# Optimization experiments

Measured on AMD Instinct MI355X. Metric: run time of the kernel, lower is better.

## Reference

```python
import jax, jax.numpy as jnp
import numpy as np

HEADS = 8


def _proj(inp, W, b):
    # 1x1 conv == per-pixel dense: W [Cout, Cin], inp [B, Cin, H, W]
    return jnp.einsum('oc,bchw->bohw', W, inp) + b[None, :, None, None]


def setup_inputs() -> dict:
    key = jax.random.key(0)
    ks = jax.random.split(key, 10)
    B, C, H, W = 2, 256, 64, 64
    s = 0.02
    return {
        'x': jax.random.normal(ks[0], (B, C, H, W), jnp.float32),
        'f_lu': jax.random.normal(ks[1], (B, C, H, W), jnp.float32),
        'Wq': jax.random.normal(ks[2], (C, C), jnp.float32) * s,
        'bq': jnp.zeros((C,), jnp.float32),
        'Wk': jax.random.normal(ks[3], (C, C), jnp.float32) * s,
        'bk': jnp.zeros((C,), jnp.float32),
        'Wv': jax.random.normal(ks[4], (C, C), jnp.float32) * s,
        'bv': jnp.zeros((C,), jnp.float32),
        'Wo': jax.random.normal(ks[5], (C, C), jnp.float32) * s,
        'bo': jnp.zeros((C,), jnp.float32),
    }


def reference(x, f_lu, Wq, bq, Wk, bk, Wv, bv, Wo, bo):
    b, c, h, w = x.shape
    heads = HEADS
    dk = c // heads
    scale = dk ** (-0.5)
    hw = h * w

    def to_heads(t):
        # [b, c, h, w] -> [b, heads, hw, dk]
        return t.reshape(b, heads, dk, hw).transpose(0, 1, 3, 2)

    q = to_heads(_proj(f_lu, Wq, bq))
    k = to_heads(_proj(x, Wk, bk))
    v = to_heads(_proj(x, Wv, bv))

    attn = jnp.einsum('bhnd,bhmd->bhnm', q, k) * scale  # [b, heads, hw, hw]
    attn = jax.nn.softmax(attn, axis=-1)
    out = jnp.einsum('bhnm,bhmd->bhnd', attn, v)  # [b, heads, hw, dk]
    out = out.transpose(0, 1, 3, 2).reshape(b, c, h, w)
    return _proj(out, Wo, bo)
```

## Files before the change

### kernel.cpp

```cpp
#include <hip/hip_runtime.h>

typedef __bf16 bf16_t;
typedef bf16_t bf16x8 __attribute__((ext_vector_type(8)));
typedef bf16_t bf16x4 __attribute__((ext_vector_type(4)));
typedef float f32x4 __attribute__((ext_vector_type(4)));

#define HW 4096
#define NC 256

__device__ __forceinline__ f32x4 mfma16(bf16x8 a, bf16x8 b, f32x4 c) {
  return __builtin_amdgcn_mfma_f32_16x16x32_bf16(a, b, c, 0, 0, 0);
}

__device__ __forceinline__ bf16x8 pack_bf16x8(float a0, float a1, float a2, float a3,
                                              float a4, float a5, float a6, float a7) {
  union { unsigned int u[4]; bf16x8 v; } r;
  asm("v_cvt_pk_bf16_f32 %0, %1, %2" : "=v"(r.u[0]) : "v"(a0), "v"(a1));
  asm("v_cvt_pk_bf16_f32 %0, %1, %2" : "=v"(r.u[1]) : "v"(a2), "v"(a3));
  asm("v_cvt_pk_bf16_f32 %0, %1, %2" : "=v"(r.u[2]) : "v"(a4), "v"(a5));
  asm("v_cvt_pk_bf16_f32 %0, %1, %2" : "=v"(r.u[3]) : "v"(a6), "v"(a7));
  return r.v;
}

__device__ __forceinline__ int kswz(int m) {
  return ((m >> 1) & 1) | (((m >> 3) & 1) << 1);
}

__global__ void cvt_w(const float* __restrict__ wq, const float* __restrict__ wk,
                      const float* __restrict__ wv, const float* __restrict__ wo,
                      bf16_t* __restrict__ dst) {
  int i = blockIdx.x * 256 + threadIdx.x;
  dst[i]          = (bf16_t)wq[i];
  dst[65536 + i]  = (bf16_t)wk[i];
  dst[131072 + i] = (bf16_t)wv[i];
  dst[196608 + i] = (bf16_t)wo[i];
}

__global__ __launch_bounds__(256) void proj_qkv(
    const float* __restrict__ x, const float* __restrict__ flu,
    const bf16_t* __restrict__ Wq, const bf16_t* __restrict__ Wk,
    const bf16_t* __restrict__ Wv,
    const float* __restrict__ bq, const float* __restrict__ bk,
    const float* __restrict__ bv,
    bf16_t* __restrict__ Qb, bf16_t* __restrict__ Kb, bf16_t* __restrict__ Vb) {
  const int p0 = blockIdx.x * 64;
  const int o0 = blockIdx.y * 64;
  const int b  = blockIdx.z;
  const int tid = threadIdx.x;
  const int w = tid >> 6;
  const int lane = tid & 63;
  const int ln = lane & 15, hi = lane >> 4;

  __shared__ __align__(16) bf16_t lds_f[64][40];
  __shared__ __align__(16) bf16_t lds_x[64][40];

  f32x4 accQ[4] = {}, accK[4] = {}, accV[4] = {};

  const int cl = tid >> 3;
  const int pp = (tid & 7) * 4;
  const float* fbase = flu + (size_t)b * NC * HW + p0;
  const float* xbase = x   + (size_t)b * NC * HW + p0;

  for (int c0 = 0; c0 < NC; c0 += 32) {
    __syncthreads();
    {
      const float* fr = fbase + (size_t)(c0 + cl) * HW;
      const float* xr = xbase + (size_t)(c0 + cl) * HW;
      float4 fa = *(const float4*)(fr + pp);
      float4 fb = *(const float4*)(fr + pp + 32);
      float4 xa = *(const float4*)(xr + pp);
      float4 xb = *(const float4*)(xr + pp + 32);
      lds_f[pp + 0][cl] = (bf16_t)fa.x;  lds_f[pp + 1][cl] = (bf16_t)fa.y;
      lds_f[pp + 2][cl] = (bf16_t)fa.z;  lds_f[pp + 3][cl] = (bf16_t)fa.w;
      lds_f[pp + 32][cl] = (bf16_t)fb.x; lds_f[pp + 33][cl] = (bf16_t)fb.y;
      lds_f[pp + 34][cl] = (bf16_t)fb.z; lds_f[pp + 35][cl] = (bf16_t)fb.w;
      lds_x[pp + 0][cl] = (bf16_t)xa.x;  lds_x[pp + 1][cl] = (bf16_t)xa.y;
      lds_x[pp + 2][cl] = (bf16_t)xa.z;  lds_x[pp + 3][cl] = (bf16_t)xa.w;
      lds_x[pp + 32][cl] = (bf16_t)xb.x; lds_x[pp + 33][cl] = (bf16_t)xb.y;
      lds_x[pp + 34][cl] = (bf16_t)xb.z; lds_x[pp + 35][cl] = (bf16_t)xb.w;
    }
    __syncthreads();

    bf16x8 af = *(const bf16x8*)&lds_f[w * 16 + ln][hi * 8];
    bf16x8 ax = *(const bf16x8*)&lds_x[w * 16 + ln][hi * 8];
    bf16x8 awv = *(const bf16x8*)(Wv + (size_t)(o0 + w * 16 + ln) * NC + c0 + hi * 8);
#pragma unroll
    for (int t = 0; t < 4; ++t) {
      bf16x8 bwq = *(const bf16x8*)(Wq + (size_t)(o0 + t * 16 + ln) * NC + c0 + hi * 8);
      accQ[t] = mfma16(af, bwq, accQ[t]);
      bf16x8 bwk = *(const bf16x8*)(Wk + (size_t)(o0 + t * 16 + ln) * NC + c0 + hi * 8);
      accK[t] = mfma16(ax, bwk, accK[t]);
      bf16x8 bx = *(const bf16x8*)&lds_x[t * 16 + ln][hi * 8];
      accV[t] = mfma16(awv, bx, accV[t]);
    }
  }

  const float scale = 0.17677669529663687f * 1.4426950408889634f;
#pragma unroll
  for (int t = 0; t < 4; ++t) {
    int o = o0 + t * 16 + ln;
    int h = o >> 5, d = o & 31;
    float bqv = bq[o], bkv = bk[o];
#pragma unroll
    for (int r = 0; r < 4; ++r) {
      int p = p0 + w * 16 + hi * 4 + r;
      size_t idx = (((size_t)(b * 8 + h)) * HW + p) * 32 + d;
      Qb[idx] = (bf16_t)((accQ[t][r] + bqv) * scale);
      Kb[idx] = (bf16_t)(accK[t][r] + bkv);
    }
  }
#pragma unroll
  for (int t = 0; t < 4; ++t) {
    int p = p0 + t * 16 + ln;
#pragma unroll
    for (int r = 0; r < 4; ++r) {
      int o = o0 + w * 16 + hi * 4 + r;
      Vb[((size_t)b * NC + o) * HW + p] = (bf16_t)(accV[t][r] + bv[o]);
    }
  }
}

__global__ __launch_bounds__(256, 2) void attn_fwd(
    const bf16_t* __restrict__ Qb, const bf16_t* __restrict__ Kb,
    const bf16_t* __restrict__ Vb, bf16_t* __restrict__ AO) {
  const int fid = blockIdx.y * 32 + blockIdx.x;
  const int lid = (fid & 7) * 64 + (fid >> 3);
  const int q0 = (lid & 31) * 128;
  const int bh = lid >> 5;
  const int b = bh >> 3, h = bh & 7;
  const int tid = threadIdx.x;
  const int w = tid >> 6, lane = tid & 63;
  const int ln = lane & 15, hi = lane >> 4;

  __shared__ __align__(16) bf16_t Kt[2][64 * 32];
  __shared__ __align__(16) bf16_t Vt[2][32 * 64];

  const bf16_t* Qh = Qb + (size_t)bh * HW * 32;
  const bf16_t* Kh = Kb + (size_t)bh * HW * 32;
  const bf16_t* Vh = Vb + ((size_t)b * NC + h * 32) * HW;

  const bf16x8 qf0 = *(const bf16x8*)(Qh + (size_t)(q0 + w * 32 + ln) * 32 + hi * 8);
  const bf16x8 qf1 = *(const bf16x8*)(Qh + (size_t)(q0 + w * 32 + 16 + ln) * 32 + hi * 8);

  f32x4 O[2][2] = {};
  f32x4 Lacc0 = {}, Lacc1 = {};
  const bf16_t one = (bf16_t)1.0f;
  const bf16x8 ones = {one, one, one, one, one, one, one, one};

  const int kr = tid >> 2, ks = tid & 3;
  const int kofs = kr * 32 + ((ks ^ kswz(kr)) * 8);
  const bf16_t* kgp = Kh + kr * 32 + ks * 8;

  const int vr = tid >> 3, vs = tid & 7;
  const int vofs = vr * 64 + ((vs ^ (vr & 7)) * 8);
  const bf16_t* vgp = Vh + (size_t)vr * HW + vs * 8;

  int kread[2][2];
  {
    const int F0 = 8 * (ln >> 2) + (ln & 3);
#pragma unroll
    for (int ch = 0; ch < 2; ++ch) {
#pragma unroll
      for (int j = 0; j < 2; ++j) {
        int row = ch * 32 + F0 + 4 * j;
        kread[ch][j] = row * 32 + ((hi ^ kswz(row)) * 8);
      }
    }
  }
  int vread[2][2];
#pragma unroll
  for (int dt = 0; dt < 2; ++dt)
#pragma unroll
    for (int ch = 0; ch < 2; ++ch)
      vread[dt][ch] = (dt * 16 + ln) * 64 + (((ch * 4 + hi) ^ (ln & 7)) * 8);

  bf16x8 kstA = *(const bf16x8*)kgp;
  bf16x8 vstA = *(const bf16x8*)vgp;
  bf16x8 kstB, vstB;

  auto compute = [&](const bf16_t* K_, const bf16_t* V_) {
    __builtin_amdgcn_s_setprio(1);
#pragma unroll
    for (int ch = 0; ch < 2; ++ch) {
      bf16x8 kf0 = *(const bf16x8*)&K_[kread[ch][0]];
      bf16x8 kf1 = *(const bf16x8*)&K_[kread[ch][1]];
      f32x4 z = {};
      f32x4 Sa0 = mfma16(kf0, qf0, z);
      f32x4 Sa1 = mfma16(kf1, qf0, z);
      f32x4 Sb0 = mfma16(kf0, qf1, z);
      f32x4 Sb1 = mfma16(kf1, qf1, z);
      float a0 = __builtin_amdgcn_exp2f(Sa0[0]), a1 = __builtin_amdgcn_exp2f(Sa0[1]);
      float a2 = __builtin_amdgcn_exp2f(Sa0[2]), a3 = __builtin_amdgcn_exp2f(Sa0[3]);
      float a4 = __builtin_amdgcn_exp2f(Sa1[0]), a5 = __builtin_amdgcn_exp2f(Sa1[1]);
      float a6 = __builtin_amdgcn_exp2f(Sa1[2]), a7 = __builtin_amdgcn_exp2f(Sa1[3]);
      float b0 = __builtin_amdgcn_exp2f(Sb0[0]), b1 = __builtin_amdgcn_exp2f(Sb0[1]);
      float b2 = __builtin_amdgcn_exp2f(Sb0[2]), b3 = __builtin_amdgcn_exp2f(Sb0[3]);
      float b4 = __builtin_amdgcn_exp2f(Sb1[0]), b5 = __builtin_amdgcn_exp2f(Sb1[1]);
      float b6 = __builtin_amdgcn_exp2f(Sb1[2]), b7 = __builtin_amdgcn_exp2f(Sb1[3]);
      bf16x8 pa = pack_bf16x8(a0, a1, a2, a3, a4, a5, a6, a7);
      bf16x8 pb = pack_bf16x8(b0, b1, b2, b3, b4, b5, b6, b7);
      Lacc0 = mfma16(ones, pa, Lacc0);
      Lacc1 = mfma16(ones, pb, Lacc1);
#pragma unroll
      for (int dt = 0; dt < 2; ++dt) {
        bf16x8 vf = *(const bf16x8*)&V_[vread[dt][ch]];
        O[0][dt] = mfma16(vf, pa, O[0][dt]);
        O[1][dt] = mfma16(vf, pb, O[1][dt]);
      }
    }
    __builtin_amdgcn_s_setprio(0);
  };

  for (int t = 0; t < 32; ++t) {
    *(bf16x8*)&Kt[0][kofs] = kstA;
    *(bf16x8*)&Vt[0][vofs] = vstA;
    __syncthreads();
    {
      kstB = *(const bf16x8*)(kgp + (size_t)(2 * t + 1) * 2048);
      vstB = *(const bf16x8*)(vgp + (2 * t + 1) * 64);
    }
    compute(Kt[0], Vt[0]);
    *(bf16x8*)&Kt[1][kofs] = kstB;
    *(bf16x8*)&Vt[1][vofs] = vstB;
    __syncthreads();
    if (t < 31) {
      kstA = *(const bf16x8*)(kgp + (size_t)(2 * t + 2) * 2048);
      vstA = *(const bf16x8*)(vgp + (2 * t + 2) * 64);
    }
    compute(Kt[1], Vt[1]);
  }

#pragma unroll
  for (int g = 0; g < 2; ++g) {
    float inv = 1.0f / (g ? Lacc1[0] : Lacc0[0]);
    const int p = q0 + w * 32 + g * 16 + ln;
#pragma unroll
    for (int dt = 0; dt < 2; ++dt) {
      f32x4 ov4 = O[g][dt];
      bf16x4 ov = {(bf16_t)(ov4[0] * inv), (bf16_t)(ov4[1] * inv),
                   (bf16_t)(ov4[2] * inv), (bf16_t)(ov4[3] * inv)};
      *(bf16x4*)(AO + ((size_t)b * HW + p) * NC + h * 32 + dt * 16 + hi * 4) = ov;
    }
  }
}

__global__ __launch_bounds__(256) void proj_out(
    const bf16_t* __restrict__ AO, const bf16_t* __restrict__ Wo,
    const float* __restrict__ bo, float* __restrict__ out) {
  const int p0 = blockIdx.x * 64;
  const int o0 = blockIdx.y * 64;
  const int b  = blockIdx.z;
  const int tid = threadIdx.x;
  const int w = tid >> 6, lane = tid & 63;
  const int ln = lane & 15, hi = lane >> 4;

  f32x4 acc[4] = {};
  for (int c0 = 0; c0 < NC; c0 += 32) {
    bf16x8 aw = *(const bf16x8*)(Wo + (size_t)(o0 + w * 16 + ln) * NC + c0 + hi * 8);
#pragma unroll
    for (int t = 0; t < 4; ++t) {
      bf16x8 bfr = *(const bf16x8*)(AO + ((size_t)b * HW + p0 + t * 16 + ln) * NC + c0 + hi * 8);
      acc[t] = mfma16(aw, bfr, acc[t]);
    }
  }
#pragma unroll
  for (int t = 0; t < 4; ++t) {
#pragma unroll
    for (int r = 0; r < 4; ++r) {
      int o = o0 + w * 16 + hi * 4 + r;
      out[((size_t)b * NC + o) * HW + p0 + t * 16 + ln] = acc[t][r] + bo[o];
    }
  }
}

extern "C" void kernel_launch(void* const* d_in, const int* in_sizes, int n_in,
                              void* d_out, int out_size, void* d_ws, size_t ws_size,
                              hipStream_t stream) {
  const float* x   = (const float*)d_in[0];
  const float* flu = (const float*)d_in[1];
  const float* Wq  = (const float*)d_in[2];
  const float* bq  = (const float*)d_in[3];
  const float* Wk  = (const float*)d_in[4];
  const float* bk  = (const float*)d_in[5];
  const float* Wv  = (const float*)d_in[6];
  const float* bv  = (const float*)d_in[7];
  const float* Wo  = (const float*)d_in[8];
  const float* bo  = (const float*)d_in[9];
  float* out = (float*)d_out;

  char* ws = (char*)d_ws;
  bf16_t* Qb = (bf16_t*)(ws);
  bf16_t* Kb = (bf16_t*)(ws + (4u << 20));
  bf16_t* Vb = (bf16_t*)(ws + (8u << 20));
  bf16_t* AO = (bf16_t*)(ws + (12u << 20));
  bf16_t* Wb = (bf16_t*)(ws + (16u << 20));

  cvt_w<<<256, 256, 0, stream>>>(Wq, Wk, Wv, Wo, Wb);
  proj_qkv<<<dim3(64, 4, 2), 256, 0, stream>>>(x, flu,
      Wb, Wb + 65536, Wb + 131072, bq, bk, bv, Qb, Kb, Vb);
  attn_fwd<<<dim3(32, 16), 256, 0, stream>>>(Qb, Kb, Vb, AO);
  proj_out<<<dim3(64, 4, 2), 256, 0, stream>>>(AO, Wb + 196608, bo, out);
}
```

Before: 92.75 us.

## Split attention key range across two wave-halves with LDS merge of partial outputs

Each attention block now handles 64 queries instead of 128, and its two pairs of waves each process half of the key/value sequence (split-K within the block). The partial O and row sums are merged through shared memory at the end. The grid grows from 512 to 1024 blocks and the launch bound asks for 4 blocks per CU, which should improve occupancy and load balance on the many CUs. The cost is more total K/V loads across blocks, because each K/V tile now serves fewer queries, plus an extra reduction step.

```diff
diff --git a/kernel.cpp b/kernel.cpp
--- a/kernel.cpp
+++ b/kernel.cpp
@@ -120,40 +120,45 @@
   }
 }
 
-__global__ __launch_bounds__(256, 2) void attn_fwd(
+__global__ __launch_bounds__(256, 4) void attn_fwd(
     const bf16_t* __restrict__ Qb, const bf16_t* __restrict__ Kb,
     const bf16_t* __restrict__ Vb, bf16_t* __restrict__ AO) {
-  const int fid = blockIdx.y * 32 + blockIdx.x;
-  const int lid = (fid & 7) * 64 + (fid >> 3);
-  const int q0 = (lid & 31) * 128;
-  const int bh = lid >> 5;
+  const int fid = blockIdx.x;
+  const int lid = (fid & 7) * 128 + (fid >> 3);
+  const int q0 = (lid & 63) * 64;
+  const int bh = lid >> 6;
   const int b = bh >> 3, h = bh & 7;
   const int tid = threadIdx.x;
   const int w = tid >> 6, lane = tid & 63;
+  const int half = w >> 1, wq = w & 1;
   const int ln = lane & 15, hi = lane >> 4;
-
-  __shared__ __align__(16) bf16_t Kt[2][64 * 32];
-  __shared__ __align__(16) bf16_t Vt[2][32 * 64];
+  const int tid_h = tid & 127;
+
+  __shared__ __align__(16) bf16_t Kt[2][2][2048];
+  __shared__ __align__(16) bf16_t Vt[2][2][2048];
 
   const bf16_t* Qh = Qb + (size_t)bh * HW * 32;
   const bf16_t* Kh = Kb + (size_t)bh * HW * 32;
   const bf16_t* Vh = Vb + ((size_t)b * NC + h * 32) * HW;
 
-  const bf16x8 qf0 = *(const bf16x8*)(Qh + (size_t)(q0 + w * 32 + ln) * 32 + hi * 8);
-  const bf16x8 qf1 = *(const bf16x8*)(Qh + (size_t)(q0 + w * 32 + 16 + ln) * 32 + hi * 8);
+  const int qb = q0 + wq * 32;
+  const bf16x8 qf0 = *(const bf16x8*)(Qh + (size_t)(qb + ln) * 32 + hi * 8);
+  const bf16x8 qf1 = *(const bf16x8*)(Qh + (size_t)(qb + 16 + ln) * 32 + hi * 8);
 
   f32x4 O[2][2] = {};
   f32x4 Lacc0 = {}, Lacc1 = {};
   const bf16_t one = (bf16_t)1.0f;
   const bf16x8 ones = {one, one, one, one, one, one, one, one};
 
-  const int kr = tid >> 2, ks = tid & 3;
-  const int kofs = kr * 32 + ((ks ^ kswz(kr)) * 8);
-  const bf16_t* kgp = Kh + kr * 32 + ks * 8;
-
-  const int vr = tid >> 3, vs = tid & 7;
-  const int vofs = vr * 64 + ((vs ^ (vr & 7)) * 8);
-  const bf16_t* vgp = Vh + (size_t)vr * HW + vs * 8;
+  const int kr = tid_h >> 1, ksp = (tid_h & 1) * 2;
+  const int kofs0 = kr * 32 + ((ksp ^ kswz(kr)) * 8);
+  const int kofs1 = kr * 32 + (((ksp + 1) ^ kswz(kr)) * 8);
+  const bf16_t* kgp = Kh + (size_t)(half * 2048 + kr) * 32 + ksp * 8;
+
+  const int vr = tid_h >> 2, vsp = (tid_h & 3) * 2;
+  const int vofs0 = vr * 64 + ((vsp ^ (vr & 7)) * 8);
+  const int vofs1 = vr * 64 + (((vsp + 1) ^ (vr & 7)) * 8);
+  const bf16_t* vgp = Vh + (size_t)vr * HW + half * 2048 + vsp * 8;
 
   int kread[2][2];
   {
@@ -174,9 +179,11 @@
     for (int ch = 0; ch < 2; ++ch)
       vread[dt][ch] = (dt * 16 + ln) * 64 + (((ch * 4 + hi) ^ (ln & 7)) * 8);
 
-  bf16x8 kstA = *(const bf16x8*)kgp;
-  bf16x8 vstA = *(const bf16x8*)vgp;
-  bf16x8 kstB, vstB;
+  bf16x8 kstA0 = *(const bf16x8*)kgp;
+  bf16x8 kstA1 = *(const bf16x8*)(kgp + 8);
+  bf16x8 vstA0 = *(const bf16x8*)vgp;
+  bf16x8 vstA1 = *(const bf16x8*)(vgp + 8);
+  bf16x8 kstB0, kstB1, vstB0, vstB1;
 
   auto compute = [&](const bf16_t* K_, const bf16_t* V_) {
     __builtin_amdgcn_s_setprio(1);
@@ -211,35 +218,73 @@
     __builtin_amdgcn_s_setprio(0);
   };
 
-  for (int t = 0; t < 32; ++t) {
-    *(bf16x8*)&Kt[0][kofs] = kstA;
-    *(bf16x8*)&Vt[0][vofs] = vstA;
+  for (int t = 0; t < 16; ++t) {
+    {
+      bf16_t* K0 = &Kt[half][0][0];
+      bf16_t* V0 = &Vt[half][0][0];
+      *(bf16x8*)&K0[kofs0] = kstA0;
+      *(bf16x8*)&K0[kofs1] = kstA1;
+      *(bf16x8*)&V0[vofs0] = vstA0;
+      *(bf16x8*)&V0[vofs1] = vstA1;
+    }
     __syncthreads();
     {
-      kstB = *(const bf16x8*)(kgp + (size_t)(2 * t + 1) * 2048);
-      vstB = *(const bf16x8*)(vgp + (2 * t + 1) * 64);
-    }
-    compute(Kt[0], Vt[0]);
-    *(bf16x8*)&Kt[1][kofs] = kstB;
-    *(bf16x8*)&Vt[1][vofs] = vstB;
+      kstB0 = *(const bf16x8*)(kgp + (size_t)(2 * t + 1) * 2048);
+      kstB1 = *(const bf16x8*)(kgp + (size_t)(2 * t + 1) * 2048 + 8);
+      vstB0 = *(const bf16x8*)(vgp + (2 * t + 1) * 64);
+      vstB1 = *(const bf16x8*)(vgp + (2 * t + 1) * 64 + 8);
+    }
+    compute(&Kt[half][0][0], &Vt[half][0][0]);
+    {
+      bf16_t* K1 = &Kt[half][1][0];
+      bf16_t* V1 = &Vt[half][1][0];
+      *(bf16x8*)&K1[kofs0] = kstB0;
+      *(bf16x8*)&K1[kofs1] = kstB1;
+      *(bf16x8*)&V1[vofs0] = vstB0;
+      *(bf16x8*)&V1[vofs1] = vstB1;
+    }
     __syncthreads();
-    if (t < 31) {
-      kstA = *(const bf16x8*)(kgp + (size_t)(2 * t + 2) * 2048);
-      vstA = *(const bf16x8*)(vgp + (2 * t + 2) * 64);
-    }
-    compute(Kt[1], Vt[1]);
-  }
-
-#pragma unroll
-  for (int g = 0; g < 2; ++g) {
-    float inv = 1.0f / (g ? Lacc1[0] : Lacc0[0]);
-    const int p = q0 + w * 32 + g * 16 + ln;
-#pragma unroll
-    for (int dt = 0; dt < 2; ++dt) {
-      f32x4 ov4 = O[g][dt];
-      bf16x4 ov = {(bf16_t)(ov4[0] * inv), (bf16_t)(ov4[1] * inv),
-                   (bf16_t)(ov4[2] * inv), (bf16_t)(ov4[3] * inv)};
-      *(bf16x4*)(AO + ((size_t)b * HW + p) * NC + h * 32 + dt * 16 + hi * 4) = ov;
+    if (t < 15) {
+      kstA0 = *(const bf16x8*)(kgp + (size_t)(2 * t + 2) * 2048);
+      kstA1 = *(const bf16x8*)(kgp + (size_t)(2 * t + 2) * 2048 + 8);
+      vstA0 = *(const bf16x8*)(vgp + (2 * t + 2) * 64);
+      vstA1 = *(const bf16x8*)(vgp + (2 * t + 2) * 64 + 8);
+    }
+    compute(&Kt[half][1][0], &Vt[half][1][0]);
+  }
+
+  __syncthreads();
+  float* MO = (float*)&Kt[0][0][0];
+  float* ML = MO + 2048;
+  if (half == 1) {
+#pragma unroll
+    for (int g = 0; g < 2; ++g) {
+      int q = wq * 32 + g * 16 + ln;
+#pragma unroll
+      for (int dt = 0; dt < 2; ++dt) {
+        int slot = dt * 4 + hi;
+        *(f32x4*)&MO[q * 32 + ((slot ^ (ln & 7)) * 4)] = O[g][dt];
+      }
+    }
+    if (hi == 0) { ML[(wq * 2 + 0) * 16 + ln] = Lacc0[0];
+                   ML[(wq * 2 + 1) * 16 + ln] = Lacc1[0]; }
+  }
+  __syncthreads();
+  if (half == 0) {
+#pragma unroll
+    for (int g = 0; g < 2; ++g) {
+      int q = wq * 32 + g * 16 + ln;
+      float l = (g ? Lacc1[0] : Lacc0[0]) + ML[(wq * 2 + g) * 16 + ln];
+      float inv = 1.0f / l;
+      const int p = q0 + q;
+#pragma unroll
+      for (int dt = 0; dt < 2; ++dt) {
+        int slot = dt * 4 + hi;
+        f32x4 o4 = O[g][dt] + *(const f32x4*)&MO[q * 32 + ((slot ^ (ln & 7)) * 4)];
+        bf16x4 ov = {(bf16_t)(o4[0] * inv), (bf16_t)(o4[1] * inv),
+                     (bf16_t)(o4[2] * inv), (bf16_t)(o4[3] * inv)};
+        *(bf16x4*)(AO + ((size_t)b * HW + p) * NC + h * 32 + dt * 16 + hi * 4) = ov;
+      }
     }
   }
 }
@@ -298,6 +343,6 @@
   cvt_w<<<256, 256, 0, stream>>>(Wq, Wk, Wv, Wo, Wb);
   proj_qkv<<<dim3(64, 4, 2), 256, 0, stream>>>(x, flu,
       Wb, Wb + 65536, Wb + 131072, bq, bk, bv, Qb, Kb, Vb);
-  attn_fwd<<<dim3(32, 16), 256, 0, stream>>>(Qb, Kb, Vb, AO);
+  attn_fwd<<<1024, 256, 0, stream>>>(Qb, Kb, Vb, AO);
   proj_out<<<dim3(64, 4, 2), 256, 0, stream>>>(AO, Wb + 196608, bo, out);
 }
```

Measured after the change: 92.62 us. About the same (-0.1%).
